# Optimization experiments

Hardware: AMD Instinct MI355X
Metric: run time of the kernel (lower is better)

Reference implementation:

```python
import jax, jax.numpy as jnp
import numpy as np

ALL_PERMS = jnp.array([[0, 1, 2], [0, 2, 1], [1, 0, 2], [1, 2, 0], [2, 0, 1], [2, 1, 0]], dtype=jnp.int32)
ENRICH_CLIP = 100.0
B, D, H = 16384, 512, 512
P_IN = D + 6 + 3   # seq_embed + pres_state(6) + round_onehot(3)
F_IN = D + 12 + 3  # seq_embed + full_state(12) + round_onehot(3)


def _gelu(x):
    return jax.nn.gelu(x, approximate=False)  # keras 'gelu' is erf-based


def _mlp3(x, w1, b1, w2, b2, w3, b3):
    h = _gelu(x @ w1 + b1)
    h = _gelu(h @ w2 + b2)
    return h @ w3 + b3


def setup_inputs() -> dict:
    key = jax.random.key(0)
    ks = jax.random.split(key, 12)
    s = 0.02
    return {
        'seq_embed': jax.random.normal(ks[0], (B, D), jnp.float32),
        'freq': jax.random.normal(ks[1], (B, 3), jnp.float32),
        'pres': (jax.random.uniform(ks[2], (B, 3)) < 0.5).astype(jnp.float32),
        'enrich': jax.random.normal(ks[3], (B, 3), jnp.float32),
        'pw1': jax.random.normal(ks[4], (P_IN, H), jnp.float32) * s, 'pb1': jnp.zeros((H,), jnp.float32),
        'pw2': jax.random.normal(ks[5], (H, H // 2), jnp.float32) * s, 'pb2': jnp.zeros((H // 2,), jnp.float32),
        'pw3': jax.random.normal(ks[6], (H // 2, 1), jnp.float32) * s, 'pb3': jnp.zeros((1,), jnp.float32),
        'fw1': jax.random.normal(ks[7], (F_IN, H), jnp.float32) * s, 'fb1': jnp.zeros((H,), jnp.float32),
        'fw2': jax.random.normal(ks[8], (H, H), jnp.float32) * s, 'fb2': jnp.zeros((H,), jnp.float32),
        'fw3': jax.random.normal(ks[9], (H, 2), jnp.float32) * s, 'fb3': jnp.zeros((2,), jnp.float32),
        'perm_idx': jax.random.randint(ks[10], (B,), 0, 6, dtype=jnp.int32),
        'round_mask': jax.random.randint(ks[11], (B, 3), 0, 2, dtype=jnp.int32),
    }


def _decode(seq_embed, freq, pres, enrich, mask_f, perms,
            pw1, pb1, pw2, pb2, pw3, pb3, fw1, fb1, fw2, fb2, fw3, fb3):
    Bn = seq_embed.shape[0]
    dt = seq_embed.dtype
    ones = jnp.ones((Bn,), dt)
    pres_state = jnp.zeros((Bn, 3, 2), dt)  # [R, (pres, decoded_flag)]
    full_state = jnp.zeros((Bn, 3, 4), dt)  # [R, (freq, pres, enrich, decoded_flag)]
    d_f = jnp.zeros((Bn, 3), dt)
    d_p = jnp.zeros((Bn, 3), dt)
    d_e = jnp.zeros((Bn, 3), dt)
    lf = lp = le = nm = jnp.float32(0.0)
    for step in range(3):
        ridx = perms[:, step]                               # [B]
        r_oh = jax.nn.one_hot(ridx, 3, dtype=dt)            # [B,3]
        take = lambda a: jnp.take_along_axis(a, ridx[:, None], axis=1)[:, 0]
        gt_f, gt_p, gt_e, m = take(freq), take(pres), take(enrich), take(mask_f)
        pres_inp = jnp.concatenate([seq_embed, pres_state.reshape(Bn, 6), r_oh], axis=1)
        pp_logit = _mlp3(pres_inp, pw1, pb1, pw2, pb2, pw3, pb3)[:, 0]
        fe_inp = jnp.concatenate([seq_embed, full_state.reshape(Bn, 12), r_oh], axis=1)
        fe_pred = _mlp3(fe_inp, fw1, fb1, fw2, fb2, fw3, fb3)
        pf, pe = fe_pred[:, 0], fe_pred[:, 1]
        lf = lf + jnp.sum(jnp.square(pf - gt_f) * m)
        bce = jnp.maximum(pp_logit, 0.0) - pp_logit * gt_p + jnp.log1p(jnp.exp(-jnp.abs(pp_logit)))
        lp = lp + jnp.sum(bce * m)
        le = le + jnp.sum(jnp.square(pe - gt_e) * m)
        nm = nm + jnp.sum(m)
        msk = m > 0.5
        act_f = jnp.where(msk, jnp.clip(pf, -10.0, 10.0), gt_f)
        act_p = jnp.where(msk, jax.nn.sigmoid(pp_logit), gt_p)
        act_e = jnp.where(msk, jnp.clip(pe, -ENRICH_CLIP, ENRICH_CLIP), gt_e)
        sel = r_oh[:, :, None]  # equal-mask scatter into the ridx-th slot
        pres_state = pres_state * (1.0 - sel) + jnp.stack([act_p, ones], axis=1)[:, None, :] * sel
        full_state = full_state * (1.0 - sel) + jnp.stack([act_f, act_p, act_e, ones], axis=1)[:, None, :] * sel
        d_f = d_f * (1.0 - r_oh) + act_f[:, None] * r_oh
        d_p = d_p * (1.0 - r_oh) + act_p[:, None] * r_oh
        d_e = d_e * (1.0 - r_oh) + act_e[:, None] * r_oh
    nm = nm + 1e-08
    return lf / nm, lp / nm, le / nm, d_f, d_p, d_e


def reference(seq_embed, freq, pres, enrich,
              pw1, pb1, pw2, pb2, pw3, pb3,
              fw1, fb1, fw2, fb2, fw3, fb3,
              perm_idx, round_mask):
    perms = ALL_PERMS[perm_idx]                      # [B,3] random round orders
    mask_f = round_mask.astype(seq_embed.dtype)      # [B,3] 0/1 mask
    lf, lp, le, d_f, d_p, d_e = _decode(seq_embed, freq, pres, enrich, mask_f, perms,
                                        pw1, pb1, pw2, pb2, pw3, pb3,
                                        fw1, fb1, fw2, fb2, fw3, fb3)
    # flat layout: [loss_freq, loss_pres, loss_enrich, dec_freq(B*3), dec_pres(B*3), dec_enrich(B*3)]
    return jnp.concatenate([jnp.stack([lf, lp, le]), d_f.ravel(), d_p.ravel(), d_e.ravel()])
```

## Files before the change

### kernel.cpp

```cpp
#include <hip/hip_runtime.h>
#include <hip/hip_bf16.h>
#include <math.h>

#define BATCH 16384

typedef unsigned short u16;
typedef short bf16x8 __attribute__((ext_vector_type(8)));
typedef float f32x4 __attribute__((ext_vector_type(4)));
typedef u16 u16x8 __attribute__((ext_vector_type(8)));
typedef u16 u16x2 __attribute__((ext_vector_type(2)));

__constant__ int PERMS_C[6][3] = {{0,1,2},{0,2,1},{1,0,2},{1,2,0},{2,0,1},{2,1,0}};

__device__ inline float bf2f(u16 u) {
    unsigned int x = ((unsigned int)u) << 16;
    float f; __builtin_memcpy(&f, &x, 4); return f;
}
__device__ inline u16 f2bf(float f) {
    __hip_bfloat16 h = __float2bfloat16(f);
    u16 u; __builtin_memcpy(&u, &h, 2); return u;
}
__device__ __forceinline__ float gelu_fast(float x) {
    float t = x * (1.59576912f + x * x * 0.07135481f);
    return x / (1.0f + __expf(-t));
}

__device__ inline void gload_lds16(const u16* g, u16* l) {
    __builtin_amdgcn_global_load_lds(
        (const __attribute__((address_space(1))) unsigned int*)g,
        (__attribute__((address_space(3))) unsigned int*)l,
        16, 0, 0);
}

__global__ __launch_bounds__(256) void prep_kernel(
    const float* __restrict__ seq,
    const float* __restrict__ pw1, const float* __restrict__ pw2,
    const float* __restrict__ fw1, const float* __restrict__ fw2,
    const float* __restrict__ pb1, const float* __restrict__ pb2,
    const float* __restrict__ fb1, const float* __restrict__ fb2,
    u16* __restrict__ sb, u16* __restrict__ W1T, u16* __restrict__ W2T,
    float* __restrict__ bias1, float* __restrict__ bias2)
{
    const int N0 = BATCH * 512;
    const int N1 = 1024 * 512;
    const int N2 = 768 * 512;
    const int N3 = 1024;
    const int N4 = 768;
    int i = blockIdx.x * 256 + threadIdx.x;
    if (i < N0) { sb[i] = f2bf(seq[i]); return; }
    i -= N0;
    if (i < N1) {
        int n = i >> 9, k = i & 511;
        float v = (n < 512) ? pw1[(size_t)k * 512 + n] : fw1[(size_t)k * 512 + (n - 512)];
        W1T[i] = f2bf(v); return;
    }
    i -= N1;
    if (i < N2) {
        int n = i >> 9, k = i & 511;
        float v = (n < 256) ? pw2[(size_t)k * 256 + n] : fw2[(size_t)k * 512 + (n - 256)];
        W2T[i] = f2bf(v); return;
    }
    i -= N2;
    if (i < N3) { bias1[i] = (i < 512) ? pb1[i] : fb1[i - 512]; return; }
    i -= N3;
    if (i < N4) { bias2[i] = (i < 256) ? pb2[i] : fb2[i - 256]; return; }
}

__global__ __launch_bounds__(256) void gemm_bf16(
    const u16* __restrict__ A, int lda,
    const u16* __restrict__ Bt, const float* __restrict__ bias,
    u16* __restrict__ C, int M, int N, int K)
{
    __shared__ __align__(16) u16 As[128 * 64];
    __shared__ __align__(16) u16 Bs[128 * 64];

    const int bm = blockIdx.x * 128;
    const int bn = blockIdx.y * 128;

    const int tid = threadIdx.x;
    const int wv = tid >> 6;
    const int lane = tid & 63;
    const int wr = wv >> 1;
    const int wc = wv & 1;

    const int lrow = lane >> 3;
    const int lcol = (lane & 7) << 3;

    f32x4 acc[4][4];
#pragma unroll
    for (int i = 0; i < 4; ++i)
#pragma unroll
        for (int j = 0; j < 4; ++j) acc[i][j] = (f32x4){0.f, 0.f, 0.f, 0.f};

    for (int k0 = 0; k0 < K; k0 += 64) {
#pragma unroll
        for (int q = 0; q < 4; ++q) {
            const int c = wv * 4 + q;
            const int row = c * 8 + lrow;
            gload_lds16(&A[(size_t)(bm + row) * lda + k0 + lcol], &As[c * 512]);
            gload_lds16(&Bt[(size_t)(bn + row) * K + k0 + lcol], &Bs[c * 512]);
        }
        __syncthreads();

#pragma unroll
        for (int ks = 0; ks < 64; ks += 32) {
            int kk = ks + (lane >> 4) * 8;
            bf16x8 af[4], bfr[4];
#pragma unroll
            for (int i = 0; i < 4; ++i)
                af[i] = *reinterpret_cast<const bf16x8*>(&As[(wr * 64 + i * 16 + (lane & 15)) * 64 + kk]);
#pragma unroll
            for (int j = 0; j < 4; ++j)
                bfr[j] = *reinterpret_cast<const bf16x8*>(&Bs[(wc * 64 + j * 16 + (lane & 15)) * 64 + kk]);
#pragma unroll
            for (int i = 0; i < 4; ++i)
#pragma unroll
                for (int j = 0; j < 4; ++j)
                    acc[i][j] = __builtin_amdgcn_mfma_f32_16x16x32_bf16(af[i], bfr[j], acc[i][j], 0, 0, 0);
        }
        __syncthreads();
    }

    const int r4 = (lane >> 4) * 4;
    const int cn = lane & 15;
#pragma unroll
    for (int i = 0; i < 4; ++i) {
#pragma unroll
        for (int j = 0; j < 4; ++j) {
            int gcol = bn + wc * 64 + j * 16 + cn;
            float bsv = bias[gcol];
#pragma unroll
            for (int r = 0; r < 4; ++r) {
                int grow = bm + wr * 64 + i * 16 + r4 + r;
                C[(size_t)grow * N + gcol] = f2bf(acc[i][j][r] + bsv);
            }
        }
    }
}


template<int NS>
__device__ __forceinline__ void h1_phase(
    const float* __restrict__ wsrc, int cw0, int rg, int row0,
    const u16* __restrict__ Z, int gcol0, char* h1base,
    const float (*state)[20], const int* rid)
{
    float w[NS + 3][2];
#pragma unroll
    for (int r = 0; r < NS + 3; ++r) {
        float2 v = *reinterpret_cast<const float2*>(&wsrc[(size_t)r * 512 + cw0]);
        w[r][0] = v.x; w[r][1] = v.y;
    }
#pragma unroll 4
    for (int r = 0; r < 16; ++r) {
        const int row = rg * 16 + r;
        const int ridx = rid[row];
        float s[NS];
        if constexpr (NS == 6) {
            float4 a = *reinterpret_cast<const float4*>(&state[row][0]);
            float2 b = *reinterpret_cast<const float2*>(&state[row][4]);
            s[0] = a.x; s[1] = a.y; s[2] = a.z; s[3] = a.w; s[4] = b.x; s[5] = b.y;
        } else {
            float4 a = *reinterpret_cast<const float4*>(&state[row][8]);
            float4 b = *reinterpret_cast<const float4*>(&state[row][12]);
            float4 c = *reinterpret_cast<const float4*>(&state[row][16]);
            s[0] = a.x; s[1] = a.y; s[2]  = a.z; s[3]  = a.w;
            s[4] = b.x; s[5] = b.y; s[6]  = b.z; s[7]  = b.w;
            s[8] = c.x; s[9] = c.y; s[10] = c.z; s[11] = c.w;
        }
        u16x2 z = *reinterpret_cast<const u16x2*>(&Z[(size_t)(row0 + row) * 1024 + gcol0]);
        float d0 = (ridx == 0) ? w[NS][0] : ((ridx == 1) ? w[NS + 1][0] : w[NS + 2][0]);
        float d1 = (ridx == 0) ? w[NS][1] : ((ridx == 1) ? w[NS + 1][1] : w[NS + 2][1]);
#pragma unroll
        for (int j = 0; j < NS; ++j) { d0 += s[j] * w[j][0]; d1 += s[j] * w[j][1]; }
        float h0 = gelu_fast(bf2f(z[0]) + d0);
        float h1 = gelu_fast(bf2f(z[1]) + d1);
        unsigned int packed = (unsigned int)f2bf(h0) | ((unsigned int)f2bf(h1) << 16);
        int byte = (row * 2048 + gcol0 * 2) ^ ((row & 7) << 4);
        *reinterpret_cast<unsigned int*>(h1base + byte) = packed;
    }
}

__global__ __launch_bounds__(1024) void decode3(
    const u16* __restrict__ Z,
    const float* __restrict__ pw1s, const float* __restrict__ fw1s,
    const u16* __restrict__ W2T, const float* __restrict__ bias2,
    const float* __restrict__ pw3, const float* __restrict__ pb3,
    const float* __restrict__ fw3, const float* __restrict__ fb3,
    const float* __restrict__ freq, const float* __restrict__ presv,
    const float* __restrict__ enrich, const int* __restrict__ round_mask,
    const int* __restrict__ perm_idx,
    float* __restrict__ part, float* __restrict__ out)
{
    __shared__ __align__(16) u16 H1s[32 * 1024];
    __shared__ float redh[16][32][3];
    __shared__ __align__(16) float state_s[32][20];
    __shared__ int pidx_s[32];
    __shared__ int rid_s[32];

    const int tid = threadIdx.x;
    const int wv  = tid >> 6;
    const int l   = tid & 63;
    const int row0 = blockIdx.x * 32;

    const int ci    = tid & 511;
    const int rg    = tid >> 9;
    const int half  = ci >> 8;
    const int cw0   = (ci & 255) * 2;
    const int gcol0 = ci * 2;
    char* h1base = reinterpret_cast<char*>(H1s);

    {
        float* ss = &state_s[0][0];
        for (int i = tid; i < 32 * 20; i += 1024) ss[i] = 0.f;
        if (tid < 32) {
            int pp = perm_idx[row0 + tid];
            pidx_s[tid] = pp;
            rid_s[tid] = PERMS_C[pp][0];
        }
    }
    __syncthreads();

    const int colbase = wv * 48;
    const bool needP = (colbase < 256);
    const bool needF = (colbase + 32) >= 256;

    float lf_acc = 0.f, bce_acc = 0.f, le_acc = 0.f, mm_acc = 0.f;

#pragma unroll 1
    for (int step = 0; step < 3; ++step) {
        asm volatile("" ::: "memory");
        if (half == 0)
            h1_phase<6>(pw1s, cw0, rg, row0, Z, gcol0, h1base, state_s, rid_s);
        else
            h1_phase<12>(fw1s, cw0, rg, row0, Z, gcol0, h1base, state_s, rid_s);
        __syncthreads();

        f32x4 acc[2][3];
#pragma unroll
        for (int rf = 0; rf < 2; ++rf)
#pragma unroll
            for (int cf = 0; cf < 3; ++cf) acc[rf][cf] = (f32x4){0.f, 0.f, 0.f, 0.f};

        const int ar = l & 15;
        const int ks = (l >> 4) * 8;
        const int swz = (ar & 7) << 4;

        if (needP) {
            for (int kf = 0; kf < 16; ++kf) {
                const int kb = (kf * 32 + ks) * 2;
                bf16x8 af0 = *reinterpret_cast<const bf16x8*>(
                    h1base + ((ar * 2048 + kb) ^ swz));
                bf16x8 af1 = *reinterpret_cast<const bf16x8*>(
                    h1base + (((16 + ar) * 2048 + kb) ^ swz));
#pragma unroll
                for (int cf = 0; cf < 3; ++cf) {
                    if (colbase + cf * 16 < 256) {
                        int col = colbase + cf * 16 + ar;
                        bf16x8 bfr = *reinterpret_cast<const bf16x8*>(
                            &W2T[(size_t)col * 512 + kf * 32 + ks]);
                        acc[0][cf] = __builtin_amdgcn_mfma_f32_16x16x32_bf16(af0, bfr, acc[0][cf], 0, 0, 0);
                        acc[1][cf] = __builtin_amdgcn_mfma_f32_16x16x32_bf16(af1, bfr, acc[1][cf], 0, 0, 0);
                    }
                }
            }
        }
        if (needF) {
            for (int kf = 0; kf < 16; ++kf) {
                const int kb = 1024 + (kf * 32 + ks) * 2;
                bf16x8 af0 = *reinterpret_cast<const bf16x8*>(
                    h1base + ((ar * 2048 + kb) ^ swz));
                bf16x8 af1 = *reinterpret_cast<const bf16x8*>(
                    h1base + (((16 + ar) * 2048 + kb) ^ swz));
#pragma unroll
                for (int cf = 0; cf < 3; ++cf) {
                    if (colbase + cf * 16 >= 256) {
                        int col = colbase + cf * 16 + ar;
                        bf16x8 bfr = *reinterpret_cast<const bf16x8*>(
                            &W2T[(size_t)col * 512 + kf * 32 + ks]);
                        acc[0][cf] = __builtin_amdgcn_mfma_f32_16x16x32_bf16(af0, bfr, acc[0][cf], 0, 0, 0);
                        acc[1][cf] = __builtin_amdgcn_mfma_f32_16x16x32_bf16(af1, bfr, acc[1][cf], 0, 0, 0);
                    }
                }
            }
        }

#pragma unroll
        for (int rf = 0; rf < 2; ++rf) {
            float hsp[4] = {0.f, 0.f, 0.f, 0.f};
            float hsf[4] = {0.f, 0.f, 0.f, 0.f};
            float hse[4] = {0.f, 0.f, 0.f, 0.f};
#pragma unroll
            for (int cf = 0; cf < 3; ++cf) {
                const int colc = colbase + cf * 16;
                const int col = colc + ar;
                const float b2 = bias2[col];
                if (colc < 256) {
                    const float w3 = pw3[col];
#pragma unroll
                    for (int g = 0; g < 4; ++g) {
                        float h = gelu_fast(acc[rf][cf][g] + b2);
                        hsp[g] += h * w3;
                    }
                } else {
                    const float wf = fw3[(col - 256) * 2];
                    const float we = fw3[(col - 256) * 2 + 1];
#pragma unroll
                    for (int g = 0; g < 4; ++g) {
                        float h = gelu_fast(acc[rf][cf][g] + b2);
                        hsf[g] += h * wf;
                        hse[g] += h * we;
                    }
                }
            }
#pragma unroll
            for (int g = 0; g < 4; ++g) {
                float a = hsp[g], b = hsf[g], c = hse[g];
#pragma unroll
                for (int m = 1; m < 16; m <<= 1) {
                    a += __shfl_xor(a, m);
                    b += __shfl_xor(b, m);
                    c += __shfl_xor(c, m);
                }
                if ((l & 15) == 0) {
                    int row = rf * 16 + (l >> 4) * 4 + g;
                    redh[wv][row][0] = a;
                    redh[wv][row][1] = b;
                    redh[wv][row][2] = c;
                }
            }
        }
        __syncthreads();

        if (wv == 0 && l < 32) {
            const int row = l;
            const int b = row0 + row;
            float sp = 0.f, sf = 0.f, se = 0.f;
#pragma unroll
            for (int w2 = 0; w2 < 16; ++w2) {
                sp += redh[w2][row][0];
                sf += redh[w2][row][1];
                se += redh[w2][row][2];
            }
            float logit = sp + pb3[0];
            float pf    = sf + fb3[0];
            float pe    = se + fb3[1];
            int ridx = rid_s[row];
            float gt_f = freq[b * 3 + ridx];
            float gt_p = presv[b * 3 + ridx];
            float gt_e = enrich[b * 3 + ridx];
            float m = (float)round_mask[b * 3 + ridx];
            lf_acc  += (pf - gt_f) * (pf - gt_f) * m;
            bce_acc += (fmaxf(logit, 0.f) - logit * gt_p + log1pf(expf(-fabsf(logit)))) * m;
            le_acc  += (pe - gt_e) * (pe - gt_e) * m;
            mm_acc  += m;
            bool msk = m > 0.5f;
            float act_f = msk ? fminf(fmaxf(pf, -10.f), 10.f) : gt_f;
            float act_p = msk ? 1.f / (1.f + expf(-logit)) : gt_p;
            float act_e = msk ? fminf(fmaxf(pe, -100.f), 100.f) : gt_e;
            state_s[row][ridx * 2 + 0] = act_p;
            state_s[row][ridx * 2 + 1] = 1.f;
            state_s[row][8 + ridx * 4 + 0] = act_f;
            state_s[row][8 + ridx * 4 + 1] = act_p;
            state_s[row][8 + ridx * 4 + 2] = act_e;
            state_s[row][8 + ridx * 4 + 3] = 1.f;
            out[3 + b * 3 + ridx] = act_f;
            out[3 + 3 * BATCH + b * 3 + ridx] = act_p;
            out[3 + 6 * BATCH + b * 3 + ridx] = act_e;
            if (step < 2) rid_s[row] = PERMS_C[pidx_s[row]][step + 1];
        }
        __syncthreads();
    }

    if (wv == 0) {
        for (int off = 32; off > 0; off >>= 1) {
            lf_acc  += __shfl_down(lf_acc, off);
            bce_acc += __shfl_down(bce_acc, off);
            le_acc  += __shfl_down(le_acc, off);
            mm_acc  += __shfl_down(mm_acc, off);
        }
        if (l == 0) {
            float4 v; v.x = lf_acc; v.y = bce_acc; v.z = le_acc; v.w = mm_acc;
            *reinterpret_cast<float4*>(&part[blockIdx.x * 4]) = v;
        }
    }
}

#define NPART (BATCH / 32)

__global__ __launch_bounds__(256) void finalize_kernel(
    const float* __restrict__ part, float* __restrict__ out)
{
    __shared__ float red[4][4];
    float a0 = 0.f, a1 = 0.f, a2 = 0.f, a3 = 0.f;
    for (int j = threadIdx.x; j < NPART; j += 256) {
        float4 v = *reinterpret_cast<const float4*>(&part[j * 4]);
        a0 += v.x; a1 += v.y; a2 += v.z; a3 += v.w;
    }
    for (int off = 32; off > 0; off >>= 1) {
        a0 += __shfl_down(a0, off);
        a1 += __shfl_down(a1, off);
        a2 += __shfl_down(a2, off);
        a3 += __shfl_down(a3, off);
    }
    const int wid = threadIdx.x >> 6, lane = threadIdx.x & 63;
    if (lane == 0) { red[wid][0] = a0; red[wid][1] = a1; red[wid][2] = a2; red[wid][3] = a3; }
    __syncthreads();
    if (threadIdx.x == 0) {
        float s0 = 0.f, s1 = 0.f, s2 = 0.f, s3 = 0.f;
#pragma unroll
        for (int w2 = 0; w2 < 4; ++w2) {
            s0 += red[w2][0]; s1 += red[w2][1]; s2 += red[w2][2]; s3 += red[w2][3];
        }
        float nm = s3 + 1e-8f;
        out[0] = s0 / nm;
        out[1] = s1 / nm;
        out[2] = s2 / nm;
    }
}

extern "C" void kernel_launch(void* const* d_in, const int* in_sizes, int n_in,
                              void* d_out, int out_size, void* d_ws, size_t ws_size,
                              hipStream_t stream)
{
    const float* seq       = (const float*)d_in[0];
    const float* freq      = (const float*)d_in[1];
    const float* presv     = (const float*)d_in[2];
    const float* enrich    = (const float*)d_in[3];
    const float* pw1       = (const float*)d_in[4];
    const float* pb1       = (const float*)d_in[5];
    const float* pw2       = (const float*)d_in[6];
    const float* pb2       = (const float*)d_in[7];
    const float* pw3       = (const float*)d_in[8];
    const float* pb3       = (const float*)d_in[9];
    const float* fw1       = (const float*)d_in[10];
    const float* fb1       = (const float*)d_in[11];
    const float* fw2       = (const float*)d_in[12];
    const float* fb2       = (const float*)d_in[13];
    const float* fw3       = (const float*)d_in[14];
    const float* fb3       = (const float*)d_in[15];
    const int*   perm_idx  = (const int*)d_in[16];
    const int*   round_mask= (const int*)d_in[17];
    float* out = (float*)d_out;

    char* w = (char*)d_ws;
    u16* sb  = (u16*)w;  w += (size_t)BATCH * 512 * 2;
    u16* Z   = (u16*)w;  w += (size_t)BATCH * 1024 * 2;
    u16* W1T = (u16*)w;  w += (size_t)1024 * 512 * 2;
    u16* W2T = (u16*)w;  w += (size_t)768 * 512 * 2;
    float* bias1 = (float*)w; w += 1024 * 4;
    float* bias2 = (float*)w; w += 768 * 4;
    float* part  = (float*)w;

    {
        const int total = BATCH * 512 + 1024 * 512 + 768 * 512 + 1024 + 768;
        int grid = (total + 255) / 256;
        prep_kernel<<<grid, 256, 0, stream>>>(seq, pw1, pw2, fw1, fw2, pb1, pb2, fb1, fb2,
                                              sb, W1T, W2T, bias1, bias2);
    }

    gemm_bf16<<<dim3(BATCH / 128, 1024 / 128), 256, 0, stream>>>(
        sb, 512, W1T, bias1, Z, BATCH, 1024, 512);

    decode3<<<NPART, 1024, 0, stream>>>(
        Z, pw1 + (size_t)512 * 512, fw1 + (size_t)512 * 512,
        W2T, bias2, pw3, pb3, fw3, fb3,
        freq, presv, enrich, round_mask, perm_idx, part, out);

    finalize_kernel<<<1, 256, 0, stream>>>(part, out);
}
```

Baseline: 434.7 us.

## Compute per-step state contribution with MFMA and stage Z tile in LDS

Replaces the scalar per-thread state-times-weight dot products in the first-layer update with a small MFMA over a padded 32-wide bf16 state/one-hot matrix and a prepacked bf16 weight slice (W1X). The block's Z tile is loaded once into LDS rather than re-read from global memory on each of the three steps. State and round one-hots are now kept in bf16, which loses precision relative to the fp32 state used before. LDS use grows by a 64KB Z tile, which may reduce occupancy.

```diff
diff --git a/kernel.cpp b/kernel.cpp
--- a/kernel.cpp
+++ b/kernel.cpp
@@ -39,13 +39,15 @@
     const float* __restrict__ pb1, const float* __restrict__ pb2,
     const float* __restrict__ fb1, const float* __restrict__ fb2,
     u16* __restrict__ sb, u16* __restrict__ W1T, u16* __restrict__ W2T,
-    float* __restrict__ bias1, float* __restrict__ bias2)
+    float* __restrict__ bias1, float* __restrict__ bias2,
+    u16* __restrict__ W1X)
 {
     const int N0 = BATCH * 512;
     const int N1 = 1024 * 512;
     const int N2 = 768 * 512;
     const int N3 = 1024;
     const int N4 = 768;
+    const int N5 = 1024 * 32;
     int i = blockIdx.x * 256 + threadIdx.x;
     if (i < N0) { sb[i] = f2bf(seq[i]); return; }
     i -= N0;
@@ -64,6 +66,20 @@
     if (i < N3) { bias1[i] = (i < 512) ? pb1[i] : fb1[i - 512]; return; }
     i -= N3;
     if (i < N4) { bias2[i] = (i < 256) ? pb2[i] : fb2[i - 256]; return; }
+    i -= N4;
+    if (i < N5) {
+        int col = i >> 5, k = i & 31;
+        float v = 0.f;
+        if (col < 512) {
+            if (k < 6)       v = pw1[(size_t)(512 + k) * 512 + col];
+            else if (k < 9)  v = pw1[(size_t)(518 + (k - 6)) * 512 + col];
+        } else {
+            int c2 = col - 512;
+            if (k >= 16 && k < 28)      v = fw1[(size_t)(512 + (k - 16)) * 512 + c2];
+            else if (k >= 28 && k < 31) v = fw1[(size_t)(524 + (k - 28)) * 512 + c2];
+        }
+        W1X[i] = f2bf(v); return;
+    }
 }
 
 __global__ __launch_bounds__(256) void gemm_bf16(
@@ -76,13 +92,11 @@
 
     const int bm = blockIdx.x * 128;
     const int bn = blockIdx.y * 128;
-
     const int tid = threadIdx.x;
     const int wv = tid >> 6;
     const int lane = tid & 63;
     const int wr = wv >> 1;
     const int wc = wv & 1;
-
     const int lrow = lane >> 3;
     const int lcol = (lane & 7) << 3;
 
@@ -138,52 +152,8 @@
     }
 }
 
-
-template<int NS>
-__device__ __forceinline__ void h1_phase(
-    const float* __restrict__ wsrc, int cw0, int rg, int row0,
-    const u16* __restrict__ Z, int gcol0, char* h1base,
-    const float (*state)[20], const int* rid)
-{
-    float w[NS + 3][2];
-#pragma unroll
-    for (int r = 0; r < NS + 3; ++r) {
-        float2 v = *reinterpret_cast<const float2*>(&wsrc[(size_t)r * 512 + cw0]);
-        w[r][0] = v.x; w[r][1] = v.y;
-    }
-#pragma unroll 4
-    for (int r = 0; r < 16; ++r) {
-        const int row = rg * 16 + r;
-        const int ridx = rid[row];
-        float s[NS];
-        if constexpr (NS == 6) {
-            float4 a = *reinterpret_cast<const float4*>(&state[row][0]);
-            float2 b = *reinterpret_cast<const float2*>(&state[row][4]);
-            s[0] = a.x; s[1] = a.y; s[2] = a.z; s[3] = a.w; s[4] = b.x; s[5] = b.y;
-        } else {
-            float4 a = *reinterpret_cast<const float4*>(&state[row][8]);
-            float4 b = *reinterpret_cast<const float4*>(&state[row][12]);
-            float4 c = *reinterpret_cast<const float4*>(&state[row][16]);
-            s[0] = a.x; s[1] = a.y; s[2]  = a.z; s[3]  = a.w;
-            s[4] = b.x; s[5] = b.y; s[6]  = b.z; s[7]  = b.w;
-            s[8] = c.x; s[9] = c.y; s[10] = c.z; s[11] = c.w;
-        }
-        u16x2 z = *reinterpret_cast<const u16x2*>(&Z[(size_t)(row0 + row) * 1024 + gcol0]);
-        float d0 = (ridx == 0) ? w[NS][0] : ((ridx == 1) ? w[NS + 1][0] : w[NS + 2][0]);
-        float d1 = (ridx == 0) ? w[NS][1] : ((ridx == 1) ? w[NS + 1][1] : w[NS + 2][1]);
-#pragma unroll
-        for (int j = 0; j < NS; ++j) { d0 += s[j] * w[j][0]; d1 += s[j] * w[j][1]; }
-        float h0 = gelu_fast(bf2f(z[0]) + d0);
-        float h1 = gelu_fast(bf2f(z[1]) + d1);
-        unsigned int packed = (unsigned int)f2bf(h0) | ((unsigned int)f2bf(h1) << 16);
-        int byte = (row * 2048 + gcol0 * 2) ^ ((row & 7) << 4);
-        *reinterpret_cast<unsigned int*>(h1base + byte) = packed;
-    }
-}
-
 __global__ __launch_bounds__(1024) void decode3(
-    const u16* __restrict__ Z,
-    const float* __restrict__ pw1s, const float* __restrict__ fw1s,
+    const u16* __restrict__ Z, const u16* __restrict__ W1X,
     const u16* __restrict__ W2T, const float* __restrict__ bias2,
     const float* __restrict__ pw3, const float* __restrict__ pb3,
     const float* __restrict__ fw3, const float* __restrict__ fb3,
@@ -192,9 +162,10 @@
     const int* __restrict__ perm_idx,
     float* __restrict__ part, float* __restrict__ out)
 {
+    __shared__ __align__(16) u16 Zs[32 * 1024];
     __shared__ __align__(16) u16 H1s[32 * 1024];
+    __shared__ __align__(16) u16 Sx[32 * 32];
     __shared__ float redh[16][32][3];
-    __shared__ __align__(16) float state_s[32][20];
     __shared__ int pidx_s[32];
     __shared__ int rid_s[32];
 
@@ -202,21 +173,29 @@
     const int wv  = tid >> 6;
     const int l   = tid & 63;
     const int row0 = blockIdx.x * 32;
-
-    const int ci    = tid & 511;
-    const int rg    = tid >> 9;
-    const int half  = ci >> 8;
-    const int cw0   = (ci & 255) * 2;
-    const int gcol0 = ci * 2;
     char* h1base = reinterpret_cast<char*>(H1s);
 
     {
-        float* ss = &state_s[0][0];
-        for (int i = tid; i < 32 * 20; i += 1024) ss[i] = 0.f;
-        if (tid < 32) {
-            int pp = perm_idx[row0 + tid];
-            pidx_s[tid] = pp;
-            rid_s[tid] = PERMS_C[pp][0];
+        const u16* zsrc = Z + (size_t)row0 * 1024;
+#pragma unroll
+        for (int q = 0; q < 4; ++q) {
+            const int c = wv * 4 + q;
+            gload_lds16(zsrc + c * 512 + l * 8, &Zs[c * 512]);
+        }
+    }
+    if (tid < 512) reinterpret_cast<unsigned int*>(Sx)[tid] = 0u;
+    if (tid < 32) {
+        int pp = perm_idx[row0 + tid];
+        pidx_s[tid] = pp;
+        rid_s[tid] = PERMS_C[pp][0];
+    }
+    __syncthreads();
+    if (tid < 32) {
+        int r0 = rid_s[tid];
+#pragma unroll
+        for (int j = 0; j < 3; ++j) {
+            Sx[tid * 32 + 6 + j]  = (j == r0) ? (u16)0x3F80 : (u16)0;
+            Sx[tid * 32 + 28 + j] = (j == r0) ? (u16)0x3F80 : (u16)0;
         }
     }
     __syncthreads();
@@ -230,10 +209,36 @@
 #pragma unroll 1
     for (int step = 0; step < 3; ++step) {
         asm volatile("" ::: "memory");
-        if (half == 0)
-            h1_phase<6>(pw1s, cw0, rg, row0, Z, gcol0, h1base, state_s, rid_s);
-        else
-            h1_phase<12>(fw1s, cw0, rg, row0, Z, gcol0, h1base, state_s, rid_s);
+        {
+            f32x4 hacc[2][4];
+#pragma unroll
+            for (int rf = 0; rf < 2; ++rf)
+#pragma unroll
+                for (int cf = 0; cf < 4; ++cf) hacc[rf][cf] = (f32x4){0.f, 0.f, 0.f, 0.f};
+            const int ar = l & 15;
+            const int ksh = (l >> 4) * 8;
+            bf16x8 sa0 = *reinterpret_cast<const bf16x8*>(&Sx[ar * 32 + ksh]);
+            bf16x8 sa1 = *reinterpret_cast<const bf16x8*>(&Sx[(16 + ar) * 32 + ksh]);
+#pragma unroll
+            for (int cf = 0; cf < 4; ++cf) {
+                int col = wv * 64 + cf * 16 + ar;
+                bf16x8 bw = *reinterpret_cast<const bf16x8*>(&W1X[col * 32 + ksh]);
+                hacc[0][cf] = __builtin_amdgcn_mfma_f32_16x16x32_bf16(sa0, bw, hacc[0][cf], 0, 0, 0);
+                hacc[1][cf] = __builtin_amdgcn_mfma_f32_16x16x32_bf16(sa1, bw, hacc[1][cf], 0, 0, 0);
+            }
+#pragma unroll
+            for (int rf = 0; rf < 2; ++rf)
+#pragma unroll
+            for (int cf = 0; cf < 4; ++cf)
+#pragma unroll
+            for (int g = 0; g < 4; ++g) {
+                int row = rf * 16 + (l >> 4) * 4 + g;
+                int col = wv * 64 + cf * 16 + ar;
+                float h = gelu_fast(bf2f(Zs[row * 1024 + col]) + hacc[rf][cf][g]);
+                int byte = (row * 2048 + col * 2) ^ ((row & 7) << 4);
+                *reinterpret_cast<u16*>(h1base + byte) = f2bf(h);
+            }
+        }
         __syncthreads();
 
         f32x4 acc[2][3];
@@ -249,16 +254,13 @@
         if (needP) {
             for (int kf = 0; kf < 16; ++kf) {
                 const int kb = (kf * 32 + ks) * 2;
-                bf16x8 af0 = *reinterpret_cast<const bf16x8*>(
-                    h1base + ((ar * 2048 + kb) ^ swz));
-                bf16x8 af1 = *reinterpret_cast<const bf16x8*>(
-                    h1base + (((16 + ar) * 2048 + kb) ^ swz));
+                bf16x8 af0 = *reinterpret_cast<const bf16x8*>(h1base + ((ar * 2048 + kb) ^ swz));
+                bf16x8 af1 = *reinterpret_cast<const bf16x8*>(h1base + (((16 + ar) * 2048 + kb) ^ swz));
 #pragma unroll
                 for (int cf = 0; cf < 3; ++cf) {
                     if (colbase + cf * 16 < 256) {
                         int col = colbase + cf * 16 + ar;
-                        bf16x8 bfr = *reinterpret_cast<const bf16x8*>(
-                            &W2T[(size_t)col * 512 + kf * 32 + ks]);
+                        bf16x8 bfr = *reinterpret_cast<const bf16x8*>(&W2T[(size_t)col * 512 + kf * 32 + ks]);
                         acc[0][cf] = __builtin_amdgcn_mfma_f32_16x16x32_bf16(af0, bfr, acc[0][cf], 0, 0, 0);
                         acc[1][cf] = __builtin_amdgcn_mfma_f32_16x16x32_bf16(af1, bfr, acc[1][cf], 0, 0, 0);
                     }
@@ -268,16 +270,13 @@
         if (needF) {
             for (int kf = 0; kf < 16; ++kf) {
                 const int kb = 1024 + (kf * 32 + ks) * 2;
-                bf16x8 af0 = *reinterpret_cast<const bf16x8*>(
-                    h1base + ((ar * 2048 + kb) ^ swz));
-                bf16x8 af1 = *reinterpret_cast<const bf16x8*>(
-                    h1base + (((16 + ar) * 2048 + kb) ^ swz));
+                bf16x8 af0 = *reinterpret_cast<const bf16x8*>(h1base + ((ar * 2048 + kb) ^ swz));
+                bf16x8 af1 = *reinterpret_cast<const bf16x8*>(h1base + (((16 + ar) * 2048 + kb) ^ swz));
 #pragma unroll
                 for (int cf = 0; cf < 3; ++cf) {
                     if (colbase + cf * 16 >= 256) {
                         int col = colbase + cf * 16 + ar;
-                        bf16x8 bfr = *reinterpret_cast<const bf16x8*>(
-                            &W2T[(size_t)col * 512 + kf * 32 + ks]);
+                        bf16x8 bfr = *reinterpret_cast<const bf16x8*>(&W2T[(size_t)col * 512 + kf * 32 + ks]);
                         acc[0][cf] = __builtin_amdgcn_mfma_f32_16x16x32_bf16(af0, bfr, acc[0][cf], 0, 0, 0);
                         acc[1][cf] = __builtin_amdgcn_mfma_f32_16x16x32_bf16(af1, bfr, acc[1][cf], 0, 0, 0);
                     }
@@ -358,16 +357,24 @@
             float act_f = msk ? fminf(fmaxf(pf, -10.f), 10.f) : gt_f;
             float act_p = msk ? 1.f / (1.f + expf(-logit)) : gt_p;
             float act_e = msk ? fminf(fmaxf(pe, -100.f), 100.f) : gt_e;
-            state_s[row][ridx * 2 + 0] = act_p;
-            state_s[row][ridx * 2 + 1] = 1.f;
-            state_s[row][8 + ridx * 4 + 0] = act_f;
-            state_s[row][8 + ridx * 4 + 1] = act_p;
-            state_s[row][8 + ridx * 4 + 2] = act_e;
-            state_s[row][8 + ridx * 4 + 3] = 1.f;
+            Sx[row * 32 + ridx * 2 + 0] = f2bf(act_p);
+            Sx[row * 32 + ridx * 2 + 1] = (u16)0x3F80;
+            Sx[row * 32 + 16 + ridx * 4 + 0] = f2bf(act_f);
+            Sx[row * 32 + 16 + ridx * 4 + 1] = f2bf(act_p);
+            Sx[row * 32 + 16 + ridx * 4 + 2] = f2bf(act_e);
+            Sx[row * 32 + 16 + ridx * 4 + 3] = (u16)0x3F80;
             out[3 + b * 3 + ridx] = act_f;
             out[3 + 3 * BATCH + b * 3 + ridx] = act_p;
             out[3 + 6 * BATCH + b * 3 + ridx] = act_e;
-            if (step < 2) rid_s[row] = PERMS_C[pidx_s[row]][step + 1];
+            if (step < 2) {
+                int rn = PERMS_C[pidx_s[row]][step + 1];
+                rid_s[row] = rn;
+#pragma unroll
+                for (int j = 0; j < 3; ++j) {
+                    Sx[row * 32 + 6 + j]  = (j == rn) ? (u16)0x3F80 : (u16)0;
+                    Sx[row * 32 + 28 + j] = (j == rn) ? (u16)0x3F80 : (u16)0;
+                }
+            }
         }
         __syncthreads();
     }
@@ -450,21 +457,21 @@
     u16* W2T = (u16*)w;  w += (size_t)768 * 512 * 2;
     float* bias1 = (float*)w; w += 1024 * 4;
     float* bias2 = (float*)w; w += 768 * 4;
+    u16* W1X = (u16*)w;  w += (size_t)1024 * 32 * 2;
     float* part  = (float*)w;
 
     {
-        const int total = BATCH * 512 + 1024 * 512 + 768 * 512 + 1024 + 768;
+        const int total = BATCH * 512 + 1024 * 512 + 768 * 512 + 1024 + 768 + 1024 * 32;
         int grid = (total + 255) / 256;
         prep_kernel<<<grid, 256, 0, stream>>>(seq, pw1, pw2, fw1, fw2, pb1, pb2, fb1, fb2,
-                                              sb, W1T, W2T, bias1, bias2);
+                                              sb, W1T, W2T, bias1, bias2, W1X);
     }
 
     gemm_bf16<<<dim3(BATCH / 128, 1024 / 128), 256, 0, stream>>>(
         sb, 512, W1T, bias1, Z, BATCH, 1024, 512);
 
     decode3<<<NPART, 1024, 0, stream>>>(
-        Z, pw1 + (size_t)512 * 512, fw1 + (size_t)512 * 512,
-        W2T, bias2, pw3, pb3, fw3, fb3,
+        Z, W1X, W2T, bias2, pw3, pb3, fw3, fb3,
         freq, presv, enrich, round_mask, perm_idx, part, out);
 
     finalize_kernel<<<1, 256, 0, stream>>>(part, out);
```

Result: faster. 407.6 us (-6.2%).
